# Kernel optimization log

Hardware: AMD Instinct MI355X
Metric: run time of the kernel (lower is better)

Reference implementation:

```python
import jax, jax.numpy as jnp
import numpy as np

RNN_NUM = 4  # rnn_num mean-field iterations


def setup_inputs() -> dict:
    key = jax.random.key(0)
    k1, k2, k3, k4 = jax.random.split(key, 4)
    T, N, M, K = 16384, 256, 8, 16  # time steps, regions, features, gaussian kernels
    inputs = jax.random.normal(k1, (T, N, M), dtype=jnp.float32)
    kernels = jax.random.uniform(k2, (N, N, K), dtype=jnp.float32)  # positive -> stable denominator
    W_feat = jax.random.uniform(k3, (1, M), dtype=jnp.float32) * 0.01  # feature_linear_layer.weight (F_in[1]=1, F_in[0]=M)
    W_lin = jax.random.uniform(k4, (1, K), dtype=jnp.float32) * 0.01   # linear_layer.weight (1, D_in)
    return {"inputs": inputs, "kernels": kernels, "W_feat": W_feat, "W_lin": W_lin}


def reference(inputs, kernels, W_feat, W_lin):
    # inputs: (T, N, M); kernels: (N, N, K); W_feat: (1, M); W_lin: (1, K)
    x = inputs @ W_feat.T                 # feature_layer -> (T, N, 1)
    originals = x
    # feature_layer(ones(T,N,M)) is constant: every entry equals sum(W_feat)
    f_weights = jnp.sum(W_feat)           # scalar, broadcasts as (T, N, 1)
    # static_conv_layer(all_ones, kernels): conv1d with length-1 input of ones
    # == row-sum of each kernel slice -> (N, K); loop-invariant, compute once.
    ones_conv = kernels.sum(axis=1)       # (N, K)
    denom = f_weights + 2.0 * (ones_conv @ W_lin.T)  # (N, 1), broadcasts over T
    for _ in range(RNN_NUM):
        # static_conv_layer(x, kernels): conv1d(length=1) == matmul per kernel slice,
        # fused over all K slices: out[t,i,k] = sum_j x[t,j] * kernels[i,j,k]
        conv = jnp.einsum('tj,ijk->tik', x[:, :, 0], kernels)  # (T, N, K)
        numer = originals + 2.0 * (conv @ W_lin.T)             # (T, N, 1)
        x = numer / denom
    return x
```

## Files before the change

### kernel.cpp

```cpp
#include <hip/hip_runtime.h>


#define NREG 256
#define KG   16
#define MF   8

typedef unsigned short u16;
typedef __attribute__((ext_vector_type(8))) short short8;
typedef __attribute__((ext_vector_type(4))) float f32x4;

__device__ __forceinline__ void async_copy16(const void* g, void* l) {
    __builtin_amdgcn_global_load_lds(
        (const __attribute__((address_space(1))) void*)g,
        (__attribute__((address_space(3))) void*)l,
        16, 0, 0);
}

__device__ __forceinline__ f32x4 ld16(const float* p) {
    f32x4 d;
    asm volatile("global_load_dwordx4 %0, %1, off" : "=v"(d) : "v"(p));
    return d;
}

__device__ __forceinline__ u16 bf16_rne(float x) {
    unsigned u = __float_as_uint(x);
    return (u16)((u + 0x7FFFu + ((u >> 16) & 1u)) >> 16);
}
__device__ __forceinline__ float bf16_to_f(u16 h) {
    return __uint_as_float(((unsigned)h) << 16);
}

__global__ __launch_bounds__(256) void k_prep(const float* __restrict__ kern,
                                              const float* __restrict__ Wlin,
                                              const float* __restrict__ Wfeat,
                                              float* __restrict__ B,
                                              float* __restrict__ Einv) {
    const int i = blockIdx.x, j = threadIdx.x;
    const float* kp = kern + ((size_t)i * NREG + j) * KG;
    float4 w0 = *(const float4*)(Wlin + 0);
    float4 w1 = *(const float4*)(Wlin + 4);
    float4 w2 = *(const float4*)(Wlin + 8);
    float4 w3 = *(const float4*)(Wlin + 12);
    float4 v0 = *(const float4*)(kp + 0);
    float4 v1 = *(const float4*)(kp + 4);
    float4 v2 = *(const float4*)(kp + 8);
    float4 v3 = *(const float4*)(kp + 12);
    float km = v0.x*w0.x + v0.y*w0.y + v0.z*w0.z + v0.w*w0.w
             + v1.x*w1.x + v1.y*w1.y + v1.z*w1.z + v1.w*w1.w
             + v2.x*w2.x + v2.y*w2.y + v2.z*w2.z + v2.w*w2.w
             + v3.x*w3.x + v3.y*w3.y + v3.z*w3.z + v3.w*w3.w;

    __shared__ float red[256];
    red[j] = km;
    __syncthreads();
    for (int s = 128; s > 0; s >>= 1) {
        if (j < s) red[j] += red[j + s];
        __syncthreads();
    }
    __shared__ float sden;
    if (j == 0) {
        float fw = 0.f;
#pragma unroll
        for (int m = 0; m < MF; ++m) fw += Wfeat[m];
        float den = fw + 2.f * red[0];
        sden = den;
        Einv[i] = 1.f / den;
    }
    __syncthreads();
    B[(size_t)i * NREG + j] = 2.f * km / sden;
}

__global__ __launch_bounds__(512) void k_rows(const float* __restrict__ B,
                                              const float* __restrict__ Einv,
                                              u16* __restrict__ Mh,
                                              u16* __restrict__ Ml) {
    const int i = blockIdx.x;
    const int j = threadIdx.x & 255;
    const int h = threadIdx.x >> 8;
    const int l0 = h * 128;
    __shared__ float rB[NREG], rP[NREG];
    __shared__ float part[2][NREG];

    if (h == 0) rB[j] = B[(size_t)i * NREG + j];
    __syncthreads();

#define ROWMM(rowv, dst_write)                                                \
    {                                                                         \
        float acc = 0.f;                                                      \
        _Pragma("unroll 4")                                                   \
        for (int l = l0; l < l0 + 128; l += 8) {                              \
            float b0 = B[(size_t)(l + 0) * NREG + j];                         \
            float b1 = B[(size_t)(l + 1) * NREG + j];                         \
            float b2 = B[(size_t)(l + 2) * NREG + j];                         \
            float b3 = B[(size_t)(l + 3) * NREG + j];                         \
            float b4 = B[(size_t)(l + 4) * NREG + j];                         \
            float b5 = B[(size_t)(l + 5) * NREG + j];                         \
            float b6 = B[(size_t)(l + 6) * NREG + j];                         \
            float b7 = B[(size_t)(l + 7) * NREG + j];                         \
            acc += rowv[l+0]*b0 + rowv[l+1]*b1 + rowv[l+2]*b2 + rowv[l+3]*b3  \
                 + rowv[l+4]*b4 + rowv[l+5]*b5 + rowv[l+6]*b6 + rowv[l+7]*b7; \
        }                                                                     \
        part[h][j] = acc;                                                     \
        __syncthreads();                                                      \
        dst_write                                                             \
        __syncthreads();                                                      \
    }

    float b2v = 0.f, b3v = 0.f, b4v = 0.f;
    ROWMM(rB,  { b2v = part[0][j] + part[1][j]; if (h == 0) rP[j] = b2v; })
    ROWMM(rP,  { b3v = part[0][j] + part[1][j]; if (h == 1) rP[j] = b3v; })
    ROWMM(rP,  { b4v = part[0][j] + part[1][j]; })

    if (h == 0) {
        const size_t idx = (size_t)i * NREG + j;
        float v = ((i == j) ? 1.f : 0.f) + rB[j] + b2v + b3v;
        v = v * Einv[j] + b4v;
        u16 hh = bf16_rne(v);
        Mh[idx] = hh;
        Ml[idx] = bf16_rne(v - bf16_to_f(hh));
    }
}

__global__ __launch_bounds__(512, 1) void k_main(const float* __restrict__ in,
                                                 const float* __restrict__ Wfeat,
                                                 const u16* __restrict__ Mh,
                                                 const u16* __restrict__ Ml,
                                                 float* __restrict__ out) {
    __shared__ __align__(16) u16 Ah[64 * 256];
    __shared__ __align__(16) u16 Al[64 * 256];
    __shared__ __align__(16) u16 Bh[256 * 64];
    __shared__ __align__(16) u16 Bl[256 * 64];

    const int tid = threadIdx.x, lane = tid & 63, wid = tid >> 6;
    const size_t t0 = (size_t)blockIdx.x * 64;

    float4 wa = *(const float4*)(Wfeat);
    float4 wb = *(const float4*)(Wfeat + 4);
    asm volatile("" :: "v"(wa.x), "v"(wa.y), "v"(wa.z), "v"(wa.w),
                       "v"(wb.x), "v"(wb.y), "v"(wb.z), "v"(wb.w));

    const float* rowbase = in + (t0 + wid * 8) * (NREG * MF);

#define ISSUE(BUF, TL)                                                        \
    {                                                                         \
        const float* rp_ = rowbase + (TL) * 2048 + lane * 8;                  \
        _Pragma("unroll")                                                     \
        for (int q = 0; q < 8; ++q)                                           \
            BUF[q] = ld16(rp_ + (q >> 1) * 512 + (q & 1) * 4);                \
    }

#define PROCESS(BUF, TL)                                                      \
    {                                                                         \
        const int t_ = wid * 8 + (TL);                                        \
        _Pragma("unroll")                                                     \
        for (int dq = 0; dq < 4; ++dq) {                                      \
            f32x4 a0 = BUF[2 * dq], a1 = BUF[2 * dq + 1];                     \
            float o = a0[0]*wa.x + a0[1]*wa.y + a0[2]*wa.z + a0[3]*wa.w       \
                    + a1[0]*wb.x + a1[1]*wb.y + a1[2]*wb.z + a1[3]*wb.w;      \
            u16 h_ = bf16_rne(o);                                             \
            u16 l_ = bf16_rne(o - bf16_to_f(h_));                             \
            const int j_ = dq * 64 + lane;                                    \
            const int idx_ = t_ * 256 + (((j_ >> 3) ^ (TL)) * 8) + (j_ & 7);  \
            Ah[idx_] = h_;                                                    \
            Al[idx_] = l_;                                                    \
        }                                                                     \
    }

#define WAITV(N)  asm volatile("s_waitcnt vmcnt(" #N ")" ::: "memory");       \
                  __builtin_amdgcn_sched_barrier(0);

    f32x4 ba[8], bb[8];
    ISSUE(ba, 0)
    ISSUE(bb, 1)
    WAITV(8)  PROCESS(ba, 0)  ISSUE(ba, 2)
    WAITV(8)  PROCESS(bb, 1)  ISSUE(bb, 3)
    WAITV(8)  PROCESS(ba, 2)  ISSUE(ba, 4)
    WAITV(8)  PROCESS(bb, 3)  ISSUE(bb, 5)
    WAITV(8)  PROCESS(ba, 4)  ISSUE(ba, 6)
    WAITV(8)  PROCESS(bb, 5)  ISSUE(bb, 7)
    WAITV(8)  PROCESS(ba, 6)
    WAITV(0)  PROCESS(bb, 7)

    __syncthreads();

    const int mrow = (wid >> 1) * 16 + (lane & 15);
    const int nh   = (wid & 1) * 8;
    f32x4 acc[8];
#pragma unroll
    for (int n = 0; n < 8; ++n) acc[n] = (f32x4){0.f, 0.f, 0.f, 0.f};

    for (int p = 0; p < 4; ++p) {
        if (p) __syncthreads();
#pragma unroll
        for (int s = 0; s < 8; ++s) {
            const int g = s * 8 + wid;
            const int i0 = (g & 31) * 8;
            const u16* sg = (g >> 5) ? Ml : Mh;
            u16* dg = (g >> 5) ? Bl : Bh;
            const int irow = i0 + (lane >> 3);
            const int ch = (lane & 7) ^ (lane >> 3);
            async_copy16(sg + (size_t)irow * NREG + p * 64 + ch * 8,
                         dg + i0 * 64);
        }
        __syncthreads();

#pragma unroll
        for (int kst = 0; kst < 2; ++kst) {
            const int achunk = (8 * p + 4 * kst + (lane >> 4)) ^ (lane & 7);
            short8 a_h = *(const short8*)(Ah + mrow * 256 + achunk * 8);
            short8 a_l = *(const short8*)(Al + mrow * 256 + achunk * 8);
#pragma unroll
            for (int n = 0; n < 8; ++n) {
                const int irow = (nh + n) * 16 + (lane & 15);
                const int bchunk = (4 * kst + (lane >> 4)) ^ (lane & 7);
                short8 b_h = *(const short8*)(Bh + irow * 64 + bchunk * 8);
                short8 b_l = *(const short8*)(Bl + irow * 64 + bchunk * 8);
                acc[n] = __builtin_amdgcn_mfma_f32_16x16x32_bf16(a_h, b_h, acc[n], 0, 0, 0);
                acc[n] = __builtin_amdgcn_mfma_f32_16x16x32_bf16(a_h, b_l, acc[n], 0, 0, 0);
                acc[n] = __builtin_amdgcn_mfma_f32_16x16x32_bf16(a_l, b_h, acc[n], 0, 0, 0);
            }
        }
    }

    const size_t tbase = t0 + (wid >> 1) * 16 + (lane >> 4) * 4;
#pragma unroll
    for (int n = 0; n < 8; ++n) {
#pragma unroll
        for (int r = 0; r < 4; ++r) {
            out[(tbase + r) * NREG + (nh + n) * 16 + (lane & 15)] = acc[n][r];
        }
    }
}

extern "C" void kernel_launch(void* const* d_in, const int* in_sizes, int n_in,
                              void* d_out, int out_size, void* d_ws, size_t ws_size,
                              hipStream_t stream) {
    const float* inputs  = (const float*)d_in[0];
    const float* kernels = (const float*)d_in[1];
    const float* Wfeat   = (const float*)d_in[2];
    const float* Wlin    = (const float*)d_in[3];
    float* out = (float*)d_out;

    float* ws   = (float*)d_ws;
    float* B    = ws;
    float* Einv = B + NREG * NREG;
    u16*   Mh   = (u16*)(Einv + NREG);
    u16*   Ml   = Mh + NREG * NREG;

    k_prep <<<256, 256, 0, stream>>>(kernels, Wlin, Wfeat, B, Einv);
    k_rows <<<256, 512, 0, stream>>>(B, Einv, Mh, Ml);
    k_main <<<256, 512, 0, stream>>>(inputs, Wfeat, Mh, Ml, out);
}
```

Before: 50.30 us.

## Halve time tile to 32 rows, launch 512 blocks with two per CU

The main kernel now processes 32 time steps per block instead of 64 and launches 512 blocks. Its launch bounds allow two blocks per CU, and LDS use drops to 64KB per block. The B staging loop is restructured into eight K-chunks of 32 with a new swizzle, and the wave-to-tile mapping changes to 2x4. The goal is more blocks in flight across the 256 CUs and better latency hiding of the streaming input load. The cost is twice as many loads of M per output and more barriers per block.

```diff
diff --git a/kernel.cpp b/kernel.cpp
--- a/kernel.cpp
+++ b/kernel.cpp
@@ -121,25 +121,25 @@
     }
 }
 
-__global__ __launch_bounds__(512, 1) void k_main(const float* __restrict__ in,
+__global__ __launch_bounds__(512, 2) void k_main(const float* __restrict__ in,
                                                  const float* __restrict__ Wfeat,
                                                  const u16* __restrict__ Mh,
                                                  const u16* __restrict__ Ml,
                                                  float* __restrict__ out) {
-    __shared__ __align__(16) u16 Ah[64 * 256];
-    __shared__ __align__(16) u16 Al[64 * 256];
-    __shared__ __align__(16) u16 Bh[256 * 64];
-    __shared__ __align__(16) u16 Bl[256 * 64];
+    __shared__ __align__(16) u16 Ah[32 * 256];
+    __shared__ __align__(16) u16 Al[32 * 256];
+    __shared__ __align__(16) u16 Bh[256 * 32];
+    __shared__ __align__(16) u16 Bl[256 * 32];
 
     const int tid = threadIdx.x, lane = tid & 63, wid = tid >> 6;
-    const size_t t0 = (size_t)blockIdx.x * 64;
+    const size_t t0 = (size_t)blockIdx.x * 32;
 
     float4 wa = *(const float4*)(Wfeat);
     float4 wb = *(const float4*)(Wfeat + 4);
     asm volatile("" :: "v"(wa.x), "v"(wa.y), "v"(wa.z), "v"(wa.w),
                        "v"(wb.x), "v"(wb.y), "v"(wb.z), "v"(wb.w));
 
-    const float* rowbase = in + (t0 + wid * 8) * (NREG * MF);
+    const float* rowbase = in + (t0 + wid * 4) * (NREG * MF);
 
 #define ISSUE(BUF, TL)                                                        \
     {                                                                         \
@@ -151,7 +151,7 @@
 
 #define PROCESS(BUF, TL)                                                      \
     {                                                                         \
-        const int t_ = wid * 8 + (TL);                                        \
+        const int t_ = wid * 4 + (TL);                                        \
         _Pragma("unroll")                                                     \
         for (int dq = 0; dq < 4; ++dq) {                                      \
             f32x4 a0 = BUF[2 * dq], a1 = BUF[2 * dq + 1];                     \
@@ -160,7 +160,7 @@
             u16 h_ = bf16_rne(o);                                             \
             u16 l_ = bf16_rne(o - bf16_to_f(h_));                             \
             const int j_ = dq * 64 + lane;                                    \
-            const int idx_ = t_ * 256 + (((j_ >> 3) ^ (TL)) * 8) + (j_ & 7);  \
+            const int idx_ = t_ * 256 + (((j_ >> 3) ^ (t_ & 7)) * 8) + (j_ & 7);\
             Ah[idx_] = h_;                                                    \
             Al[idx_] = l_;                                                    \
         }                                                                     \
@@ -174,60 +174,62 @@
     ISSUE(bb, 1)
     WAITV(8)  PROCESS(ba, 0)  ISSUE(ba, 2)
     WAITV(8)  PROCESS(bb, 1)  ISSUE(bb, 3)
-    WAITV(8)  PROCESS(ba, 2)  ISSUE(ba, 4)
-    WAITV(8)  PROCESS(bb, 3)  ISSUE(bb, 5)
-    WAITV(8)  PROCESS(ba, 4)  ISSUE(ba, 6)
-    WAITV(8)  PROCESS(bb, 5)  ISSUE(bb, 7)
-    WAITV(8)  PROCESS(ba, 6)
-    WAITV(0)  PROCESS(bb, 7)
-
-    __syncthreads();
-
-    const int mrow = (wid >> 1) * 16 + (lane & 15);
-    const int nh   = (wid & 1) * 8;
-    f32x4 acc[8];
-#pragma unroll
-    for (int n = 0; n < 8; ++n) acc[n] = (f32x4){0.f, 0.f, 0.f, 0.f};
-
-    for (int p = 0; p < 4; ++p) {
-        if (p) __syncthreads();
-#pragma unroll
-        for (int s = 0; s < 8; ++s) {
-            const int g = s * 8 + wid;
-            const int i0 = (g & 31) * 8;
-            const u16* sg = (g >> 5) ? Ml : Mh;
-            u16* dg = (g >> 5) ? Bl : Bh;
-            const int irow = i0 + (lane >> 3);
-            const int ch = (lane & 7) ^ (lane >> 3);
-            async_copy16(sg + (size_t)irow * NREG + p * 64 + ch * 8,
-                         dg + i0 * 64);
+    WAITV(8)  PROCESS(ba, 2)
+    WAITV(0)  PROCESS(bb, 3)
+
+    __syncthreads();
+
+    const int m  = wid >> 2, nq = wid & 3;
+    const int mrow = m * 16 + (lane & 15);
+    f32x4 acc[4];
+#pragma unroll
+    for (int n = 0; n < 4; ++n) acc[n] = (f32x4){0.f, 0.f, 0.f, 0.f};
+
+#define STAGEB(P)                                                             \
+    {                                                                         \
+        _Pragma("unroll")                                                     \
+        for (int s2 = 0; s2 < 4; ++s2) {                                      \
+            const int i0r = (s2 * 8 + wid) * 8;                               \
+            const int irow = i0r + (lane >> 2);                               \
+            const int sc = (lane & 3) ^ ((lane >> 2) & 3);                    \
+            async_copy16(Mh + (size_t)irow * NREG + (P) * 32 + sc * 8,        \
+                         Bh + i0r * 32);                                      \
+            async_copy16(Ml + (size_t)irow * NREG + (P) * 32 + sc * 8,        \
+                         Bl + i0r * 32);                                      \
+        }                                                                     \
+    }
+
+    const int bcs = (lane >> 4) ^ (lane & 3);
+
+    STAGEB(0)
+    __syncthreads();
+
+    for (int p = 0; p < 8; ++p) {
+        const int achunk = (p * 4 + (lane >> 4)) ^ (lane & 7);
+        short8 a_h = *(const short8*)(Ah + mrow * 256 + achunk * 8);
+        short8 a_l = *(const short8*)(Al + mrow * 256 + achunk * 8);
+#pragma unroll
+        for (int n = 0; n < 4; ++n) {
+            const int irow = (nq * 4 + n) * 16 + (lane & 15);
+            short8 b_h = *(const short8*)(Bh + irow * 32 + bcs * 8);
+            short8 b_l = *(const short8*)(Bl + irow * 32 + bcs * 8);
+            acc[n] = __builtin_amdgcn_mfma_f32_16x16x32_bf16(a_h, b_h, acc[n], 0, 0, 0);
+            acc[n] = __builtin_amdgcn_mfma_f32_16x16x32_bf16(a_h, b_l, acc[n], 0, 0, 0);
+            acc[n] = __builtin_amdgcn_mfma_f32_16x16x32_bf16(a_l, b_h, acc[n], 0, 0, 0);
         }
-        __syncthreads();
-
-#pragma unroll
-        for (int kst = 0; kst < 2; ++kst) {
-            const int achunk = (8 * p + 4 * kst + (lane >> 4)) ^ (lane & 7);
-            short8 a_h = *(const short8*)(Ah + mrow * 256 + achunk * 8);
-            short8 a_l = *(const short8*)(Al + mrow * 256 + achunk * 8);
-#pragma unroll
-            for (int n = 0; n < 8; ++n) {
-                const int irow = (nh + n) * 16 + (lane & 15);
-                const int bchunk = (4 * kst + (lane >> 4)) ^ (lane & 7);
-                short8 b_h = *(const short8*)(Bh + irow * 64 + bchunk * 8);
-                short8 b_l = *(const short8*)(Bl + irow * 64 + bchunk * 8);
-                acc[n] = __builtin_amdgcn_mfma_f32_16x16x32_bf16(a_h, b_h, acc[n], 0, 0, 0);
-                acc[n] = __builtin_amdgcn_mfma_f32_16x16x32_bf16(a_h, b_l, acc[n], 0, 0, 0);
-                acc[n] = __builtin_amdgcn_mfma_f32_16x16x32_bf16(a_l, b_h, acc[n], 0, 0, 0);
-            }
+        if (p < 7) {
+            __syncthreads();
+            STAGEB(p + 1)
+            __syncthreads();
         }
     }
 
-    const size_t tbase = t0 + (wid >> 1) * 16 + (lane >> 4) * 4;
-#pragma unroll
-    for (int n = 0; n < 8; ++n) {
+    const size_t tbase = t0 + m * 16 + (lane >> 4) * 4;
+#pragma unroll
+    for (int n = 0; n < 4; ++n) {
 #pragma unroll
         for (int r = 0; r < 4; ++r) {
-            out[(tbase + r) * NREG + (nh + n) * 16 + (lane & 15)] = acc[n][r];
+            out[(tbase + r) * NREG + (nq * 4 + n) * 16 + (lane & 15)] = acc[n][r];
         }
     }
 }
@@ -249,5 +251,5 @@
 
     k_prep <<<256, 256, 0, stream>>>(kernels, Wlin, Wfeat, B, Einv);
     k_rows <<<256, 512, 0, stream>>>(B, Einv, Mh, Ml);
-    k_main <<<256, 512, 0, stream>>>(inputs, Wfeat, Mh, Ml, out);
-}
+    k_main <<<512, 512, 0, stream>>>(inputs, Wfeat, Mh, Ml, out);
+}
```

Result: slower. 53.10 us (+5.6%).

## Fuse prep, row and main kernels into one cooperative kernel with grid syncs

Applied to the files above, without the earlier changes.

Merges the three launches into a single cooperative kernel that uses grid.sync() between the kernel-reduction, matrix-power and main GEMM phases. The input load and bf16 conversion for the main phase now run after the row phase and before the second grid sync, so they overlap with other blocks finishing the matrix build. This removes launch gaps and inter-kernel drains. In exchange it adds grid-wide barrier cost, requires all 256 blocks to be co-resident, and raises LDS use per block.

```diff
diff --git a/kernel.cpp b/kernel.cpp
--- a/kernel.cpp
+++ b/kernel.cpp
@@ -1,4 +1,7 @@
 #include <hip/hip_runtime.h>
+#include <hip/hip_cooperative_groups.h>
+
+namespace cg = cooperative_groups;
 
 
 #define NREG 256
@@ -30,59 +33,70 @@
     return __uint_as_float(((unsigned)h) << 16);
 }
 
-__global__ __launch_bounds__(256) void k_prep(const float* __restrict__ kern,
-                                              const float* __restrict__ Wlin,
-                                              const float* __restrict__ Wfeat,
-                                              float* __restrict__ B,
-                                              float* __restrict__ Einv) {
-    const int i = blockIdx.x, j = threadIdx.x;
-    const float* kp = kern + ((size_t)i * NREG + j) * KG;
-    float4 w0 = *(const float4*)(Wlin + 0);
-    float4 w1 = *(const float4*)(Wlin + 4);
-    float4 w2 = *(const float4*)(Wlin + 8);
-    float4 w3 = *(const float4*)(Wlin + 12);
-    float4 v0 = *(const float4*)(kp + 0);
-    float4 v1 = *(const float4*)(kp + 4);
-    float4 v2 = *(const float4*)(kp + 8);
-    float4 v3 = *(const float4*)(kp + 12);
-    float km = v0.x*w0.x + v0.y*w0.y + v0.z*w0.z + v0.w*w0.w
-             + v1.x*w1.x + v1.y*w1.y + v1.z*w1.z + v1.w*w1.w
-             + v2.x*w2.x + v2.y*w2.y + v2.z*w2.z + v2.w*w2.w
-             + v3.x*w3.x + v3.y*w3.y + v3.z*w3.z + v3.w*w3.w;
-
-    __shared__ float red[256];
-    red[j] = km;
+__global__ __launch_bounds__(512, 1)
+void k_all(const float* __restrict__ in,
+           const float* __restrict__ kern,
+           const float* __restrict__ Wfeat,
+           const float* __restrict__ Wlin,
+           float* __restrict__ B,
+           float* __restrict__ Einv,
+           u16* __restrict__ Mh,
+           u16* __restrict__ Ml,
+           float* __restrict__ out) {
+    __shared__ __align__(16) u16 Ah[64 * 256];
+    __shared__ __align__(16) u16 Al[64 * 256];
+    __shared__ __align__(16) u16 Bh[256 * 64];
+    __shared__ __align__(16) u16 Bl[256 * 64];
+    __shared__ float red[NREG];
+    __shared__ float rB[NREG], rP[NREG];
+    __shared__ float part[2][NREG];
+    __shared__ float sden;
+
+    const int tid = threadIdx.x, lane = tid & 63, wid = tid >> 6;
+    const int b = blockIdx.x;
+    const int j = tid & 255;
+    const int h = tid >> 8;
+    cg::grid_group grid = cg::this_grid();
+
+    float km = 0.f;
+    if (h == 0) {
+        const float* kp = kern + ((size_t)b * NREG + j) * KG;
+        float4 w0 = *(const float4*)(Wlin + 0);
+        float4 w1 = *(const float4*)(Wlin + 4);
+        float4 w2 = *(const float4*)(Wlin + 8);
+        float4 w3 = *(const float4*)(Wlin + 12);
+        float4 v0 = *(const float4*)(kp + 0);
+        float4 v1 = *(const float4*)(kp + 4);
+        float4 v2 = *(const float4*)(kp + 8);
+        float4 v3 = *(const float4*)(kp + 12);
+        km = v0.x*w0.x + v0.y*w0.y + v0.z*w0.z + v0.w*w0.w
+           + v1.x*w1.x + v1.y*w1.y + v1.z*w1.z + v1.w*w1.w
+           + v2.x*w2.x + v2.y*w2.y + v2.z*w2.z + v2.w*w2.w
+           + v3.x*w3.x + v3.y*w3.y + v3.z*w3.z + v3.w*w3.w;
+        red[j] = km;
+    }
     __syncthreads();
     for (int s = 128; s > 0; s >>= 1) {
-        if (j < s) red[j] += red[j + s];
+        if (h == 0 && j < s) red[j] += red[j + s];
         __syncthreads();
     }
-    __shared__ float sden;
-    if (j == 0) {
+    if (tid == 0) {
         float fw = 0.f;
 #pragma unroll
         for (int m = 0; m < MF; ++m) fw += Wfeat[m];
         float den = fw + 2.f * red[0];
         sden = den;
-        Einv[i] = 1.f / den;
+        Einv[b] = 1.f / den;
     }
     __syncthreads();
-    B[(size_t)i * NREG + j] = 2.f * km / sden;
-}
-
-__global__ __launch_bounds__(512) void k_rows(const float* __restrict__ B,
-                                              const float* __restrict__ Einv,
-                                              u16* __restrict__ Mh,
-                                              u16* __restrict__ Ml) {
-    const int i = blockIdx.x;
-    const int j = threadIdx.x & 255;
-    const int h = threadIdx.x >> 8;
-    const int l0 = h * 128;
-    __shared__ float rB[NREG], rP[NREG];
-    __shared__ float part[2][NREG];
-
-    if (h == 0) rB[j] = B[(size_t)i * NREG + j];
-    __syncthreads();
+    if (h == 0) B[(size_t)b * NREG + j] = 2.f * km / sden;
+
+    grid.sync();
+
+    {
+        const int l0 = h * 128;
+        if (h == 0) rB[j] = B[(size_t)b * NREG + j];
+        __syncthreads();
 
 #define ROWMM(rowv, dst_write)                                                \
     {                                                                         \
@@ -106,34 +120,22 @@
         __syncthreads();                                                      \
     }
 
-    float b2v = 0.f, b3v = 0.f, b4v = 0.f;
-    ROWMM(rB,  { b2v = part[0][j] + part[1][j]; if (h == 0) rP[j] = b2v; })
-    ROWMM(rP,  { b3v = part[0][j] + part[1][j]; if (h == 1) rP[j] = b3v; })
-    ROWMM(rP,  { b4v = part[0][j] + part[1][j]; })
-
-    if (h == 0) {
-        const size_t idx = (size_t)i * NREG + j;
-        float v = ((i == j) ? 1.f : 0.f) + rB[j] + b2v + b3v;
-        v = v * Einv[j] + b4v;
-        u16 hh = bf16_rne(v);
-        Mh[idx] = hh;
-        Ml[idx] = bf16_rne(v - bf16_to_f(hh));
-    }
-}
-
-__global__ __launch_bounds__(512, 1) void k_main(const float* __restrict__ in,
-                                                 const float* __restrict__ Wfeat,
-                                                 const u16* __restrict__ Mh,
-                                                 const u16* __restrict__ Ml,
-                                                 float* __restrict__ out) {
-    __shared__ __align__(16) u16 Ah[64 * 256];
-    __shared__ __align__(16) u16 Al[64 * 256];
-    __shared__ __align__(16) u16 Bh[256 * 64];
-    __shared__ __align__(16) u16 Bl[256 * 64];
-
-    const int tid = threadIdx.x, lane = tid & 63, wid = tid >> 6;
-    const size_t t0 = (size_t)blockIdx.x * 64;
-
+        float b2v = 0.f, b3v = 0.f, b4v = 0.f;
+        ROWMM(rB,  { b2v = part[0][j] + part[1][j]; if (h == 0) rP[j] = b2v; })
+        ROWMM(rP,  { b3v = part[0][j] + part[1][j]; if (h == 1) rP[j] = b3v; })
+        ROWMM(rP,  { b4v = part[0][j] + part[1][j]; })
+
+        if (h == 0) {
+            const size_t idx = (size_t)b * NREG + j;
+            float v = ((b == j) ? 1.f : 0.f) + rB[j] + b2v + b3v;
+            v = v * Einv[j] + b4v;
+            u16 hh = bf16_rne(v);
+            Mh[idx] = hh;
+            Ml[idx] = bf16_rne(v - bf16_to_f(hh));
+        }
+    }
+
+    const size_t t0 = (size_t)b * 64;
     float4 wa = *(const float4*)(Wfeat);
     float4 wb = *(const float4*)(Wfeat + 4);
     asm volatile("" :: "v"(wa.x), "v"(wa.y), "v"(wa.z), "v"(wa.w),
@@ -182,9 +184,11 @@
     WAITV(0)  PROCESS(bb, 7)
 
     __syncthreads();
-
-    const int mrow = (wid >> 1) * 16 + (lane & 15);
-    const int nh   = (wid & 1) * 8;
+    grid.sync();
+
+    const int m  = wid >> 1;
+    const int nh = (wid & 1) * 8;
+    const int mrow = m * 16 + (lane & 15);
     f32x4 acc[8];
 #pragma unroll
     for (int n = 0; n < 8; ++n) acc[n] = (f32x4){0.f, 0.f, 0.f, 0.f};
@@ -222,7 +226,7 @@
         }
     }
 
-    const size_t tbase = t0 + (wid >> 1) * 16 + (lane >> 4) * 4;
+    const size_t tbase = t0 + m * 16 + (lane >> 4) * 4;
 #pragma unroll
     for (int n = 0; n < 8; ++n) {
 #pragma unroll
@@ -247,7 +251,10 @@
     u16*   Mh   = (u16*)(Einv + NREG);
     u16*   Ml   = Mh + NREG * NREG;
 
-    k_prep <<<256, 256, 0, stream>>>(kernels, Wlin, Wfeat, B, Einv);
-    k_rows <<<256, 512, 0, stream>>>(B, Einv, Mh, Ml);
-    k_main <<<256, 512, 0, stream>>>(inputs, Wfeat, Mh, Ml, out);
-}
+    void* args[] = {
+        (void*)&inputs, (void*)&kernels, (void*)&Wfeat, (void*)&Wlin,
+        (void*)&B, (void*)&Einv, (void*)&Mh, (void*)&Ml, (void*)&out
+    };
+    hipLaunchCooperativeKernel((void*)k_all, dim3(256), dim3(512),
+                               args, 0, stream);
+}
```

Result: slower. 113.5 us (+125.6%).
